# Kernel tuning notes

Measured on AMD Instinct MI355X. Metric: run time of the kernel, lower is better.

The kernel has to match this reference:

```python
import jax, jax.numpy as jnp
import numpy as np

D_MODEL = 1024
HEADS = 16
D_K = D_MODEL // HEADS
THETA = 10000.0
NEG = -1.0e9


def _rope(t, offset=0):
    # t: [B, H, S, D]; standard interleaved rotary embedding, base THETA
    S, D = t.shape[-2], t.shape[-1]
    half = D // 2
    inv_freq = 1.0 / (THETA ** (jnp.arange(half, dtype=jnp.float32) * 2.0 / D))
    pos = jnp.arange(offset, offset + S, dtype=jnp.float32)
    ang = pos[:, None] * inv_freq[None, :]          # [S, half]
    cos, sin = jnp.cos(ang), jnp.sin(ang)
    t1, t2 = t[..., ::2], t[..., 1::2]              # even / odd lanes
    o1 = t1 * cos - t2 * sin
    o2 = t1 * sin + t2 * cos
    return jnp.stack([o1, o2], axis=-1).reshape(t.shape)


def setup_inputs() -> dict:
    key = jax.random.key(0)
    k0, k1, k2, k3, k4 = jax.random.split(key, 5)
    B, S = 2, 2048
    x = jax.random.normal(k0, (B, S, D_MODEL), dtype=jnp.float32)
    att_mask = jnp.ones((B, S), dtype=jnp.int32)
    scale = 0.02
    wq = jax.random.normal(k1, (D_MODEL, D_MODEL), dtype=jnp.float32) * scale
    wk = jax.random.normal(k2, (D_MODEL, D_MODEL), dtype=jnp.float32) * scale
    wv = jax.random.normal(k3, (D_MODEL, D_MODEL), dtype=jnp.float32) * scale
    wo = jax.random.normal(k4, (D_MODEL, D_MODEL), dtype=jnp.float32) * scale
    return {"x": x, "att_mask": att_mask, "wq": wq, "wk": wk, "wv": wv, "wo": wo}


def reference(x, att_mask, wq, wk, wv, wo):
    B, S, _ = x.shape
    # nn.Linear(bias=False): y = x @ W^T ; then split heads -> [B, H, S, d_k]
    q = (x @ wq.T).reshape(B, S, HEADS, D_K).transpose(0, 2, 1, 3)
    k = (x @ wk.T).reshape(B, S, HEADS, D_K).transpose(0, 2, 1, 3)
    v = (x @ wv.T).reshape(B, S, HEADS, D_K).transpose(0, 2, 1, 3)
    # use_rope=True, start_pos=0, use_cache=False path
    q = _rope(q)
    k = _rope(k)
    scores = jnp.einsum("bhqd,bhkd->bhqk", q, k) / np.sqrt(D_K).astype(np.float32)
    pad = (att_mask == 0)[:, None, None, :]          # [B,1,1,S]
    scores = jnp.where(pad, NEG, scores)
    causal = jnp.tril(jnp.ones((S, S), dtype=bool))  # [S, S]
    scores = jnp.where(causal, scores, NEG)
    att = jax.nn.softmax(scores, axis=-1)
    ctx = jnp.einsum("bhqk,bhkd->bhqd", att, v)      # [B,H,S,d_k]
    final = ctx.transpose(0, 2, 1, 3).reshape(B, S, HEADS * D_K)
    return final @ wo.T
```

## Files before the change

kernel.cpp:

```cpp
#include <hip/hip_runtime.h>
#include <hip/hip_bf16.h>
#include <cstdint>

typedef unsigned short u16;
typedef __bf16 bf16x8 __attribute__((ext_vector_type(8)));
typedef float f32x4 __attribute__((ext_vector_type(4)));

#define S_LEN 2048
#define NH 16
#define DK 64
#define DM 1024

__device__ __forceinline__ u16 f2bf(float f) {
  union { float f; uint32_t u; } c; c.f = f;
  uint32_t u = c.u;
  u += 0x7fffu + ((u >> 16) & 1u);
  return (u16)(u >> 16);
}

__device__ __forceinline__ void gl_lds16(const void* gsrc, void* ldst) {
  __builtin_amdgcn_global_load_lds(
      (const __attribute__((address_space(1))) unsigned int*)gsrc,
      (__attribute__((address_space(3))) unsigned int*)ldst,
      16, 0, 0);
}

#define MFMA16(a, b, c) __builtin_amdgcn_mfma_f32_16x16x32_bf16((a), (b), (c), 0, 0, 0)
#define VMW(N) asm volatile("s_waitcnt vmcnt(" #N ")" ::: "memory")
#define BARM() asm volatile("s_barrier" ::: "memory")

__global__ __launch_bounds__(256) void convert_all(
    const float* x, const float* wq, const float* wk, const float* wv, const float* wo,
    u16* xb, u16* wqb, u16* wkb, u16* wvb, u16* wob)
{
  size_t i = ((size_t)blockIdx.x * 256 + threadIdx.x) * 4;
  const float* src; u16* dst; size_t off;
  if (i < 4194304u)      { src = x;  dst = xb;  off = i; }
  else if (i < 5242880u) { src = wq; dst = wqb; off = i - 4194304u; }
  else if (i < 6291456u) { src = wk; dst = wkb; off = i - 5242880u; }
  else if (i < 7340032u) { src = wv; dst = wvb; off = i - 6291456u; }
  else                   { src = wo; dst = wob; off = i - 7340032u; }
  float4 v = *(const float4*)(src + off);
  ushort4 o;
  o.x = f2bf(v.x); o.y = f2bf(v.y); o.z = f2bf(v.z); o.w = f2bf(v.w);
  *(ushort4*)(dst + off) = o;
}

__global__ __launch_bounds__(256) void rope_tab_k(float2* tab) {
  int i = blockIdx.x * 256 + threadIdx.x;
  int pos = i >> 5, f = i & 31;
  float inv = powf(10000.0f, -(float)f / 32.0f);
  float ang = (float)pos * inv;
  tab[i] = make_float2(cosf(ang), sinf(ang));
}

__global__ __launch_bounds__(64) void mask_flags(const int* amask, int* mflag) {
  const int f = blockIdx.x;
  const int b = f >> 5, t = f & 31;
  int v = amask[b * S_LEN + t * 64 + threadIdx.x];
  int all = (int)__all(v != 0);
  if (threadIdx.x == 0) mflag[f] = all;
}

__global__ __launch_bounds__(512, 2) void gemm_qkv8(
    const u16* xb, const u16* wqb, const u16* wkb, const u16* wvb,
    const float2* tab, u16* Qr, u16* Kr, u16* Vt)
{
  __shared__ __align__(16) u16 lds[2][2][2][128 * 64];

  const int bid = blockIdx.x;
  const int xcd = bid & 7, v = bid >> 3;
  const int mt = xcd * 2 + (v >= 12 ? 1 : 0);
  const int nt = (v >= 12) ? v - 12 : v;
  const int m0 = mt * 256;
  const int z = nt >> 2;
  const int n0z = (nt & 3) * 256;
  const u16* Wz = (z == 0) ? wqb : ((z == 1) ? wkb : wvb);

  const int tid = threadIdx.x;
  const int w8 = tid >> 6, lane = tid & 63;
  const int wm = w8 >> 2, wn = w8 & 3;
  const int l15 = lane & 15, g = lane >> 4;
  const int swb = ((lane & 7) * 16) ^ (((lane >> 3) & 7) << 4);

  f32x4 acc[8][4] = {};
  bf16x8 aF[2][4][2];
  bf16x8 bC[2][2];

  auto stageA = [&](int buf, int h, int kt) {
#pragma unroll
    for (int i = 0; i < 2; ++i) {
      const int rb = i * 64 + w8 * 8;
      const int row = rb + (lane >> 3);
      gl_lds16((const char*)(xb + (size_t)(m0 + h * 128 + row) * DM + kt * 64) + swb,
               (char*)&lds[buf][0][h][0] + rb * 128);
    }
  };
  auto stageB = [&](int buf, int h, int kt) {
#pragma unroll
    for (int i = 0; i < 2; ++i) {
      const int rb = i * 64 + w8 * 8;
      const int row = rb + (lane >> 3);
      gl_lds16((const char*)(Wz + (size_t)(n0z + h * 128 + row) * DM + kt * 64) + swb,
               (char*)&lds[buf][1][h][0] + rb * 128);
    }
  };
  auto loadA = [&](int cur, int mi) {
#pragma unroll
    for (int f = 0; f < 4; ++f) {
      const int row = wm * 64 + f * 16 + l15;
#pragma unroll
      for (int kk = 0; kk < 2; ++kk)
        aF[mi][f][kk] = *(const bf16x8*)((const char*)&lds[cur][0][mi][0] + row * 128 +
                                         ((kk * 64 + g * 16) ^ ((row & 7) << 4)));
    }
  };
  auto loadB = [&](int cur, int ni) {
#pragma unroll
    for (int f = 0; f < 2; ++f) {
      const int row = wn * 32 + f * 16 + l15;
#pragma unroll
      for (int kk = 0; kk < 2; ++kk)
        bC[f][kk] = *(const bf16x8*)((const char*)&lds[cur][1][ni][0] + row * 128 +
                                     ((kk * 64 + g * 16) ^ ((row & 7) << 4)));
    }
  };
  auto quad = [&](int mi, int ni) {
    __builtin_amdgcn_s_setprio(1);
#pragma unroll
    for (int f = 0; f < 4; ++f)
#pragma unroll
      for (int f2 = 0; f2 < 2; ++f2)
#pragma unroll
        for (int kk = 0; kk < 2; ++kk)
          acc[mi * 4 + f][ni * 2 + f2] =
              MFMA16(aF[mi][f][kk], bC[f2][kk], acc[mi * 4 + f][ni * 2 + f2]);
    __builtin_amdgcn_s_setprio(0);
  };

  stageA(0, 0, 0); stageB(0, 0, 0); stageA(0, 1, 0); stageB(0, 1, 0);

  for (int kt = 0; kt < 16; ++kt) {
    const int cur = kt & 1, nx = cur ^ 1;
    const bool pf = (kt < 15);
    if (pf) { stageA(nx, 0, kt + 1); VMW(6); } else { VMW(4); }
    BARM();
    loadA(cur, 0); loadB(cur, 0);
    quad(0, 0);
    if (pf) { stageB(nx, 0, kt + 1); VMW(6); } else { VMW(2); }
    BARM();
    loadA(cur, 1);
    quad(1, 0);
    if (pf) { stageA(nx, 1, kt + 1); VMW(6); } else { VMW(0); }
    BARM();
    loadB(cur, 1);
    quad(0, 1);
    if (pf) { stageB(nx, 1, kt + 1); VMW(6); }
    BARM();
    quad(1, 1);
  }

#pragma unroll
  for (int fm = 0; fm < 8; ++fm) {
    const int mrow = m0 + (fm >> 2) * 128 + wm * 64 + (fm & 3) * 16 + g * 4;
#pragma unroll
    for (int fn = 0; fn < 4; ++fn) {
      const int col = n0z + (fn >> 1) * 128 + wn * 32 + (fn & 1) * 16 + l15;
      const int h = col >> 6, d = col & 63;
#pragma unroll
      for (int r = 0; r < 4; ++r) {
        const int m = mrow + r;
        const int b = m >> 11, s = m & 2047;
        float vv = acc[fm][fn][r];
        if (z < 2) {
          float p = __shfl_xor(vv, 1);
          float2 cs = tab[s * 32 + (d >> 1)];
          float o = vv * cs.x + ((d & 1) ? p : -p) * cs.y;
          if (z == 0) o *= 0.125f;
          u16* dst = (z == 0) ? Qr : Kr;
          dst[((size_t)(b * NH + h) * S_LEN + s) * DK + d] = f2bf(o);
        } else {
          Vt[((size_t)(b * NH + h) * DK + d) * S_LEN + s] = f2bf(vv);
        }
      }
    }
  }
}

__device__ __forceinline__ void xcd_map(int bid, int& m0, int& n0) {
  const int xcd = bid & 7, v = bid >> 3;
  m0 = (xcd * 4 + (v >> 3)) * 128;
  n0 = (v & 7) * 128;
}

__global__ __launch_bounds__(256) void gemm_out(const u16* ctx, const u16* wob, float* out) {
  __shared__ __align__(16) u16 ldsA[2][128 * 64];
  __shared__ __align__(16) u16 ldsB[2][128 * 64];
  int m0, n0;
  xcd_map(blockIdx.x, m0, n0);

  const int tid = threadIdx.x;
  const int w = tid >> 6, lane = tid & 63;
  const int l15 = lane & 15, g = lane >> 4;
  const int wm = (w >> 1) * 64, wn = (w & 1) * 64;
  const int lrow = lane >> 3;
  const int scolb = ((lane & 7) * 16) ^ (lrow << 4);
  f32x4 acc[4][4] = {};

  auto stage = [&](int buf, int kt) {
#pragma unroll
    for (int c = 0; c < 4; ++c) {
      const int rb = w * 32 + c * 8;
      const int row = rb + lrow;
      gl_lds16((const char*)(ctx + (size_t)(m0 + row) * DM + kt) + scolb,
               (char*)&ldsA[buf][0] + rb * 128);
      gl_lds16((const char*)(wob + (size_t)(n0 + row) * DM + kt) + scolb,
               (char*)&ldsB[buf][0] + rb * 128);
    }
  };

  stage(0, 0);
  int cur = 0;
  for (int kt = 0; kt < DM; kt += 64) {
    if (kt + 64 < DM) { stage(cur ^ 1, kt + 64); VMW(8); } else { VMW(0); }
    BARM();
#pragma unroll
    for (int ks = 0; ks < 2; ++ks) {
      bf16x8 af[4], bfr[4];
#pragma unroll
      for (int i = 0; i < 4; ++i) {
        const int ar = wm + i * 16 + l15;
        af[i] = *(const bf16x8*)((const char*)&ldsA[cur][0] + ar * 128 +
                                 ((ks * 64 + g * 16) ^ ((ar & 7) << 4)));
        const int br = wn + i * 16 + l15;
        bfr[i] = *(const bf16x8*)((const char*)&ldsB[cur][0] + br * 128 +
                                  ((ks * 64 + g * 16) ^ ((br & 7) << 4)));
      }
      __builtin_amdgcn_s_setprio(1);
#pragma unroll
      for (int i = 0; i < 4; ++i)
#pragma unroll
        for (int j = 0; j < 4; ++j)
          acc[i][j] = MFMA16(af[i], bfr[j], acc[i][j]);
      __builtin_amdgcn_s_setprio(0);
    }
    BARM();
    cur ^= 1;
  }

#pragma unroll
  for (int i = 0; i < 4; ++i)
#pragma unroll
    for (int j = 0; j < 4; ++j)
#pragma unroll
      for (int r = 0; r < 4; ++r)
        out[(size_t)(m0 + wm + i * 16 + g * 4 + r) * DM + n0 + wn + j * 16 + l15] = acc[i][j][r];
}

__global__ __launch_bounds__(512, 4) void attn9(
    const u16* Qr, const u16* Kr, const u16* Vt, const int* amask, const int* mflag,
    u16* ctx)
{
  __shared__ __align__(16) u16 ldsK[2][64 * 64];
  __shared__ __align__(16) u16 ldsV[2][64 * 64];
  __shared__ __align__(16) __bf16 plds[8][16 * 72];

  const int bh = blockIdx.x;
  const int grp = 15 - blockIdx.y;
  const int b = bh >> 4, h = bh & 15;
  const int tid = threadIdx.x, w8 = tid >> 6, lane = tid & 63;
  const int l15 = lane & 15, g = lane >> 4;
  const int r8 = lane >> 3;
  const int sw = ((lane & 7) * 16) ^ (r8 << 4);

  const int chunk = grp * 4 + (w8 >> 1);
  const int q0 = chunk * 32 + (w8 & 1) * 16;
  const int myNt = (chunk >> 1) + 1;
  const int dTile = chunk >> 1;
  const int ntB = grp * 2 + 2;

  const u16* Kb0 = Kr + (size_t)bh * S_LEN * DK;
  const u16* Vb0 = Vt + (size_t)bh * DK * S_LEN;
  const u16* Qb  = Qr + (size_t)bh * S_LEN * DK;

  bf16x8 qa0 = *(const bf16x8*)(Qb + (size_t)(q0 + l15) * DK + g * 8);
  bf16x8 qa1 = *(const bf16x8*)(Qb + (size_t)(q0 + l15) * DK + 32 + g * 8);

  union { u16 u[8]; bf16x8 v; } one_u;
#pragma unroll
  for (int i = 0; i < 8; ++i) one_u.u[i] = 0x3F80;
  const bf16x8 ones = one_u.v;

  float m[4];
  f32x4 lacc = {0.f, 0.f, 0.f, 0.f};
  f32x4 o[4];
#pragma unroll
  for (int r = 0; r < 4; ++r) m[r] = -3e38f;
#pragma unroll
  for (int dt = 0; dt < 4; ++dt) o[dt] = (f32x4){0.f, 0.f, 0.f, 0.f};

  auto stage = [&](int buf, int t) {
    const size_t kv0 = (size_t)t * 64;
    const int row = w8 * 8 + r8;
    gl_lds16((const char*)(Kb0 + (kv0 + row) * DK) + sw,
             (char*)&ldsK[buf][0] + (w8 * 8) * 128);
    gl_lds16((const char*)(Vb0 + (size_t)row * S_LEN + kv0) + sw,
             (char*)&ldsV[buf][0] + (w8 * 8) * 128);
  };

  stage(0, 0);
  int cur = 0;

  for (int t = 0; t < ntB; ++t) {
    if (t + 1 < ntB) { stage(cur ^ 1, t + 1); VMW(2); } else { VMW(0); }
    BARM();
    if (t < myNt) {
      const int kv0 = t * 64;
      const bool allok = mflag[(b << 5) + t] != 0;

      bf16x8 kb[4][2];
#pragma unroll
      for (int nt = 0; nt < 4; ++nt) {
        const int row = nt * 16 + l15;
#pragma unroll
        for (int ks = 0; ks < 2; ++ks)
          kb[nt][ks] = *(const bf16x8*)((const char*)&ldsK[cur][0] + row * 128 +
                                        ((ks * 64 + g * 16) ^ ((row & 7) << 4)));
      }
      f32x4 s[4];
#pragma unroll
      for (int nt = 0; nt < 4; ++nt) s[nt] = (f32x4){0.f, 0.f, 0.f, 0.f};
      __builtin_amdgcn_s_setprio(1);
#pragma unroll
      for (int nt = 0; nt < 4; ++nt) {
        s[nt] = MFMA16(qa0, kb[nt][0], s[nt]);
        s[nt] = MFMA16(qa1, kb[nt][1], s[nt]);
      }
      __builtin_amdgcn_s_setprio(0);

      if (!allok) {
#pragma unroll
        for (int nt = 0; nt < 4; ++nt) {
          const int pmv = amask[b * S_LEN + kv0 + nt * 16 + l15];
#pragma unroll
          for (int r = 0; r < 4; ++r)
            if (!pmv) s[nt][r] = -1e9f;
        }
      }
      if (t == dTile) {
#pragma unroll
        for (int nt = 0; nt < 4; ++nt) {
          const int kvc = kv0 + nt * 16 + l15;
#pragma unroll
          for (int r = 0; r < 4; ++r)
            s[nt][r] = (kvc <= q0 + g * 4 + r) ? s[nt][r] : -1e9f;
        }
      }

      float tmax[4];
      bool need = false;
#pragma unroll
      for (int r = 0; r < 4; ++r) {
        float t0 = fmaxf(fmaxf(s[0][r], s[1][r]), fmaxf(s[2][r], s[3][r]));
        t0 = fmaxf(t0, __shfl_xor(t0, 1));
        t0 = fmaxf(t0, __shfl_xor(t0, 2));
        t0 = fmaxf(t0, __shfl_xor(t0, 4));
        t0 = fmaxf(t0, __shfl_xor(t0, 8));
        tmax[r] = t0;
        need = need || (t0 > m[r] + 8.f);
      }
      if (__any((int)need)) {
#pragma unroll
        for (int r = 0; r < 4; ++r) {
          const float mnew = fmaxf(m[r], tmax[r]);
          const float alpha = __expf(m[r] - mnew);
          m[r] = mnew;
          lacc[r] *= alpha;
#pragma unroll
          for (int dt = 0; dt < 4; ++dt) o[dt][r] *= alpha;
        }
      }
      __bf16* pw = &plds[w8][0];
#pragma unroll
      for (int r = 0; r < 4; ++r) {
#pragma unroll
        for (int nt = 0; nt < 4; ++nt)
          pw[(g * 4 + r) * 72 + nt * 16 + l15] = (__bf16)__expf(s[nt][r] - m[r]);
      }
      bf16x8 pa0 = *(const bf16x8*)(pw + l15 * 72 + g * 8);
      bf16x8 pa1 = *(const bf16x8*)(pw + l15 * 72 + 32 + g * 8);
      bf16x8 vb[4][2];
#pragma unroll
      for (int dt = 0; dt < 4; ++dt) {
        const int row = dt * 16 + l15;
#pragma unroll
        for (int ks = 0; ks < 2; ++ks)
          vb[dt][ks] = *(const bf16x8*)((const char*)&ldsV[cur][0] + row * 128 +
                                        ((ks * 64 + g * 16) ^ ((row & 7) << 4)));
      }
      __builtin_amdgcn_s_setprio(1);
      lacc = MFMA16(pa0, ones, lacc);
      lacc = MFMA16(pa1, ones, lacc);
#pragma unroll
      for (int dt = 0; dt < 4; ++dt) {
        o[dt] = MFMA16(pa0, vb[dt][0], o[dt]);
        o[dt] = MFMA16(pa1, vb[dt][1], o[dt]);
      }
      __builtin_amdgcn_s_setprio(0);
    }
    BARM();
    cur ^= 1;
  }

#pragma unroll
  for (int dt = 0; dt < 4; ++dt)
#pragma unroll
    for (int r = 0; r < 4; ++r) {
      const int q = q0 + g * 4 + r;
      ctx[((size_t)(b * S_LEN + q)) * DM + h * DK + dt * 16 + l15] =
          f2bf(o[dt][r] / lacc[r]);
    }
}

extern "C" void kernel_launch(void* const* d_in, const int* in_sizes, int n_in,
                              void* d_out, int out_size, void* d_ws, size_t ws_size,
                              hipStream_t stream) {
  const float* x   = (const float*)d_in[0];
  const int* amask = (const int*)d_in[1];
  const float* wq  = (const float*)d_in[2];
  const float* wk  = (const float*)d_in[3];
  const float* wv  = (const float*)d_in[4];
  const float* wo  = (const float*)d_in[5];
  float* out = (float*)d_out;

  char* ws = (char*)d_ws;
  u16* xb    = (u16*)(ws);
  u16* wqb   = (u16*)(ws + ( 8u << 20));
  u16* wkb   = (u16*)(ws + (10u << 20));
  u16* wvb   = (u16*)(ws + (12u << 20));
  u16* wob   = (u16*)(ws + (14u << 20));
  float2* tab = (float2*)(ws + (16u << 20));
  int* mflag = (int*)(ws + (16u << 20) + (768u << 10));
  u16* Qr    = (u16*)(ws + (17u << 20));
  u16* Kr    = (u16*)(ws + (25u << 20));
  u16* Vt    = (u16*)(ws + (33u << 20));
  u16* ctx   = (u16*)(ws + (41u << 20));

  hipLaunchKernelGGL(convert_all, dim3(8192), dim3(256), 0, stream,
                     x, wq, wk, wv, wo, xb, wqb, wkb, wvb, wob);
  hipLaunchKernelGGL(rope_tab_k, dim3(256), dim3(256), 0, stream, tab);
  hipLaunchKernelGGL(mask_flags, dim3(64), dim3(64), 0, stream, amask, mflag);
  hipLaunchKernelGGL(gemm_qkv8, dim3(192), dim3(512), 0, stream,
                     xb, wqb, wkb, wvb, tab, Qr, Kr, Vt);
  hipLaunchKernelGGL(attn9, dim3(32, 16), dim3(512), 0, stream,
                     Qr, Kr, Vt, amask, mflag, ctx);
  hipLaunchKernelGGL(gemm_out, dim3(256), dim3(256), 0, stream, ctx, wob, out);
}
```

Measured before the change: 149.9 us.

## Use 128x128 tiles for QKV GEMM and 32-row query blocks per attention wave

The QKV projection changes from 256x256 tiles on 512-thread blocks (192 blocks) to 128x128 tiles on 256-thread blocks (768 blocks), reusing the gemm_out main loop. Attention moves from 8 waves of 16 query rows each to 4 waves of 32 query rows each, so every K/V fragment loaded from LDS feeds two query sets. The aim is better K/V reuse in attention and better CU fill in the GEMM. In exchange, each GEMM block reuses less data per tile, and attention needs more registers per wave and runs fewer waves.

New measurement: 178.1 us. 1.19x slower.

```diff
diff --git a/kernel.cpp b/kernel.cpp
--- a/kernel.cpp
+++ b/kernel.cpp
@@ -62,142 +62,20 @@
   if (threadIdx.x == 0) mflag[f] = all;
 }
 
-__global__ __launch_bounds__(512, 2) void gemm_qkv8(
+__global__ __launch_bounds__(256) void gemm_qkv128(
     const u16* xb, const u16* wqb, const u16* wkb, const u16* wvb,
     const float2* tab, u16* Qr, u16* Kr, u16* Vt)
 {
-  __shared__ __align__(16) u16 lds[2][2][2][128 * 64];
+  __shared__ __align__(16) u16 ldsA[2][128 * 64];
+  __shared__ __align__(16) u16 ldsB[2][128 * 64];
 
   const int bid = blockIdx.x;
   const int xcd = bid & 7, v = bid >> 3;
-  const int mt = xcd * 2 + (v >= 12 ? 1 : 0);
-  const int nt = (v >= 12) ? v - 12 : v;
-  const int m0 = mt * 256;
-  const int z = nt >> 2;
-  const int n0z = (nt & 3) * 256;
+  const int m0 = (xcd * 4 + (v & 3)) * 128;
+  const int nc = v >> 2;
+  const int z = nc >> 3;
+  const int n0z = (nc & 7) * 128;
   const u16* Wz = (z == 0) ? wqb : ((z == 1) ? wkb : wvb);
-
-  const int tid = threadIdx.x;
-  const int w8 = tid >> 6, lane = tid & 63;
-  const int wm = w8 >> 2, wn = w8 & 3;
-  const int l15 = lane & 15, g = lane >> 4;
-  const int swb = ((lane & 7) * 16) ^ (((lane >> 3) & 7) << 4);
-
-  f32x4 acc[8][4] = {};
-  bf16x8 aF[2][4][2];
-  bf16x8 bC[2][2];
-
-  auto stageA = [&](int buf, int h, int kt) {
-#pragma unroll
-    for (int i = 0; i < 2; ++i) {
-      const int rb = i * 64 + w8 * 8;
-      const int row = rb + (lane >> 3);
-      gl_lds16((const char*)(xb + (size_t)(m0 + h * 128 + row) * DM + kt * 64) + swb,
-               (char*)&lds[buf][0][h][0] + rb * 128);
-    }
-  };
-  auto stageB = [&](int buf, int h, int kt) {
-#pragma unroll
-    for (int i = 0; i < 2; ++i) {
-      const int rb = i * 64 + w8 * 8;
-      const int row = rb + (lane >> 3);
-      gl_lds16((const char*)(Wz + (size_t)(n0z + h * 128 + row) * DM + kt * 64) + swb,
-               (char*)&lds[buf][1][h][0] + rb * 128);
-    }
-  };
-  auto loadA = [&](int cur, int mi) {
-#pragma unroll
-    for (int f = 0; f < 4; ++f) {
-      const int row = wm * 64 + f * 16 + l15;
-#pragma unroll
-      for (int kk = 0; kk < 2; ++kk)
-        aF[mi][f][kk] = *(const bf16x8*)((const char*)&lds[cur][0][mi][0] + row * 128 +
-                                         ((kk * 64 + g * 16) ^ ((row & 7) << 4)));
-    }
-  };
-  auto loadB = [&](int cur, int ni) {
-#pragma unroll
-    for (int f = 0; f < 2; ++f) {
-      const int row = wn * 32 + f * 16 + l15;
-#pragma unroll
-      for (int kk = 0; kk < 2; ++kk)
-        bC[f][kk] = *(const bf16x8*)((const char*)&lds[cur][1][ni][0] + row * 128 +
-                                     ((kk * 64 + g * 16) ^ ((row & 7) << 4)));
-    }
-  };
-  auto quad = [&](int mi, int ni) {
-    __builtin_amdgcn_s_setprio(1);
-#pragma unroll
-    for (int f = 0; f < 4; ++f)
-#pragma unroll
-      for (int f2 = 0; f2 < 2; ++f2)
-#pragma unroll
-        for (int kk = 0; kk < 2; ++kk)
-          acc[mi * 4 + f][ni * 2 + f2] =
-              MFMA16(aF[mi][f][kk], bC[f2][kk], acc[mi * 4 + f][ni * 2 + f2]);
-    __builtin_amdgcn_s_setprio(0);
-  };
-
-  stageA(0, 0, 0); stageB(0, 0, 0); stageA(0, 1, 0); stageB(0, 1, 0);
-
-  for (int kt = 0; kt < 16; ++kt) {
-    const int cur = kt & 1, nx = cur ^ 1;
-    const bool pf = (kt < 15);
-    if (pf) { stageA(nx, 0, kt + 1); VMW(6); } else { VMW(4); }
-    BARM();
-    loadA(cur, 0); loadB(cur, 0);
-    quad(0, 0);
-    if (pf) { stageB(nx, 0, kt + 1); VMW(6); } else { VMW(2); }
-    BARM();
-    loadA(cur, 1);
-    quad(1, 0);
-    if (pf) { stageA(nx, 1, kt + 1); VMW(6); } else { VMW(0); }
-    BARM();
-    loadB(cur, 1);
-    quad(0, 1);
-    if (pf) { stageB(nx, 1, kt + 1); VMW(6); }
-    BARM();
-    quad(1, 1);
-  }
-
-#pragma unroll
-  for (int fm = 0; fm < 8; ++fm) {
-    const int mrow = m0 + (fm >> 2) * 128 + wm * 64 + (fm & 3) * 16 + g * 4;
-#pragma unroll
-    for (int fn = 0; fn < 4; ++fn) {
-      const int col = n0z + (fn >> 1) * 128 + wn * 32 + (fn & 1) * 16 + l15;
-      const int h = col >> 6, d = col & 63;
-#pragma unroll
-      for (int r = 0; r < 4; ++r) {
-        const int m = mrow + r;
-        const int b = m >> 11, s = m & 2047;
-        float vv = acc[fm][fn][r];
-        if (z < 2) {
-          float p = __shfl_xor(vv, 1);
-          float2 cs = tab[s * 32 + (d >> 1)];
-          float o = vv * cs.x + ((d & 1) ? p : -p) * cs.y;
-          if (z == 0) o *= 0.125f;
-          u16* dst = (z == 0) ? Qr : Kr;
-          dst[((size_t)(b * NH + h) * S_LEN + s) * DK + d] = f2bf(o);
-        } else {
-          Vt[((size_t)(b * NH + h) * DK + d) * S_LEN + s] = f2bf(vv);
-        }
-      }
-    }
-  }
-}
-
-__device__ __forceinline__ void xcd_map(int bid, int& m0, int& n0) {
-  const int xcd = bid & 7, v = bid >> 3;
-  m0 = (xcd * 4 + (v >> 3)) * 128;
-  n0 = (v & 7) * 128;
-}
-
-__global__ __launch_bounds__(256) void gemm_out(const u16* ctx, const u16* wob, float* out) {
-  __shared__ __align__(16) u16 ldsA[2][128 * 64];
-  __shared__ __align__(16) u16 ldsB[2][128 * 64];
-  int m0, n0;
-  xcd_map(blockIdx.x, m0, n0);
 
   const int tid = threadIdx.x;
   const int w = tid >> 6, lane = tid & 63;
@@ -212,9 +90,9 @@
     for (int c = 0; c < 4; ++c) {
       const int rb = w * 32 + c * 8;
       const int row = rb + lrow;
-      gl_lds16((const char*)(ctx + (size_t)(m0 + row) * DM + kt) + scolb,
+      gl_lds16((const char*)(xb + (size_t)(m0 + row) * DM + kt) + scolb,
                (char*)&ldsA[buf][0] + rb * 128);
-      gl_lds16((const char*)(wob + (size_t)(n0 + row) * DM + kt) + scolb,
+      gl_lds16((const char*)(Wz + (size_t)(n0z + row) * DM + kt) + scolb,
                (char*)&ldsB[buf][0] + rb * 128);
     }
   };
@@ -248,6 +126,93 @@
     cur ^= 1;
   }
 
+  u16* dst = (z == 0) ? Qr : Kr;
+#pragma unroll
+  for (int i = 0; i < 4; ++i) {
+#pragma unroll
+    for (int j = 0; j < 4; ++j) {
+      const int n = n0z + wn + j * 16 + l15;
+      const int h = n >> 6, d = n & 63;
+#pragma unroll
+      for (int r = 0; r < 4; ++r) {
+        const int m = m0 + wm + i * 16 + g * 4 + r;
+        const int b = m >> 11, s = m & 2047;
+        float vv = acc[i][j][r];
+        if (z < 2) {
+          float p = __shfl_xor(vv, 1);
+          float2 cs = tab[s * 32 + (d >> 1)];
+          float o = vv * cs.x + ((d & 1) ? p : -p) * cs.y;
+          if (z == 0) o *= 0.125f;
+          dst[((size_t)(b * NH + h) * S_LEN + s) * DK + d] = f2bf(o);
+        } else {
+          Vt[((size_t)(b * NH + h) * DK + d) * S_LEN + s] = f2bf(vv);
+        }
+      }
+    }
+  }
+}
+
+__device__ __forceinline__ void xcd_map(int bid, int& m0, int& n0) {
+  const int xcd = bid & 7, v = bid >> 3;
+  m0 = (xcd * 4 + (v >> 3)) * 128;
+  n0 = (v & 7) * 128;
+}
+
+__global__ __launch_bounds__(256) void gemm_out(const u16* ctx, const u16* wob, float* out) {
+  __shared__ __align__(16) u16 ldsA[2][128 * 64];
+  __shared__ __align__(16) u16 ldsB[2][128 * 64];
+  int m0, n0;
+  xcd_map(blockIdx.x, m0, n0);
+
+  const int tid = threadIdx.x;
+  const int w = tid >> 6, lane = tid & 63;
+  const int l15 = lane & 15, g = lane >> 4;
+  const int wm = (w >> 1) * 64, wn = (w & 1) * 64;
+  const int lrow = lane >> 3;
+  const int scolb = ((lane & 7) * 16) ^ (lrow << 4);
+  f32x4 acc[4][4] = {};
+
+  auto stage = [&](int buf, int kt) {
+#pragma unroll
+    for (int c = 0; c < 4; ++c) {
+      const int rb = w * 32 + c * 8;
+      const int row = rb + lrow;
+      gl_lds16((const char*)(ctx + (size_t)(m0 + row) * DM + kt) + scolb,
+               (char*)&ldsA[buf][0] + rb * 128);
+      gl_lds16((const char*)(wob + (size_t)(n0 + row) * DM + kt) + scolb,
+               (char*)&ldsB[buf][0] + rb * 128);
+    }
+  };
+
+  stage(0, 0);
+  int cur = 0;
+  for (int kt = 0; kt < DM; kt += 64) {
+    if (kt + 64 < DM) { stage(cur ^ 1, kt + 64); VMW(8); } else { VMW(0); }
+    BARM();
+#pragma unroll
+    for (int ks = 0; ks < 2; ++ks) {
+      bf16x8 af[4], bfr[4];
+#pragma unroll
+      for (int i = 0; i < 4; ++i) {
+        const int ar = wm + i * 16 + l15;
+        af[i] = *(const bf16x8*)((const char*)&ldsA[cur][0] + ar * 128 +
+                                 ((ks * 64 + g * 16) ^ ((ar & 7) << 4)));
+        const int br = wn + i * 16 + l15;
+        bfr[i] = *(const bf16x8*)((const char*)&ldsB[cur][0] + br * 128 +
+                                  ((ks * 64 + g * 16) ^ ((br & 7) << 4)));
+      }
+      __builtin_amdgcn_s_setprio(1);
+#pragma unroll
+      for (int i = 0; i < 4; ++i)
+#pragma unroll
+        for (int j = 0; j < 4; ++j)
+          acc[i][j] = MFMA16(af[i], bfr[j], acc[i][j]);
+      __builtin_amdgcn_s_setprio(0);
+    }
+    BARM();
+    cur ^= 1;
+  }
+
 #pragma unroll
   for (int i = 0; i < 4; ++i)
 #pragma unroll
@@ -257,62 +222,73 @@
         out[(size_t)(m0 + wm + i * 16 + g * 4 + r) * DM + n0 + wn + j * 16 + l15] = acc[i][j][r];
 }
 
-__global__ __launch_bounds__(512, 4) void attn9(
+__global__ __launch_bounds__(256) void attn10(
     const u16* Qr, const u16* Kr, const u16* Vt, const int* amask, const int* mflag,
     u16* ctx)
 {
   __shared__ __align__(16) u16 ldsK[2][64 * 64];
   __shared__ __align__(16) u16 ldsV[2][64 * 64];
-  __shared__ __align__(16) __bf16 plds[8][16 * 72];
+  __shared__ __align__(16) __bf16 plds[4][32 * 72];
 
   const int bh = blockIdx.x;
-  const int grp = 15 - blockIdx.y;
+  const int band = 15 - blockIdx.y;
   const int b = bh >> 4, h = bh & 15;
-  const int tid = threadIdx.x, w8 = tid >> 6, lane = tid & 63;
+  const int tid = threadIdx.x, w = tid >> 6, lane = tid & 63;
   const int l15 = lane & 15, g = lane >> 4;
   const int r8 = lane >> 3;
   const int sw = ((lane & 7) * 16) ^ (r8 << 4);
 
-  const int chunk = grp * 4 + (w8 >> 1);
-  const int q0 = chunk * 32 + (w8 & 1) * 16;
+  const int chunk = band * 4 + w;
+  const int q0 = chunk * 32;
   const int myNt = (chunk >> 1) + 1;
   const int dTile = chunk >> 1;
-  const int ntB = grp * 2 + 2;
+  const int ntB = band * 2 + 2;
 
   const u16* Kb0 = Kr + (size_t)bh * S_LEN * DK;
   const u16* Vb0 = Vt + (size_t)bh * DK * S_LEN;
   const u16* Qb  = Qr + (size_t)bh * S_LEN * DK;
 
-  bf16x8 qa0 = *(const bf16x8*)(Qb + (size_t)(q0 + l15) * DK + g * 8);
-  bf16x8 qa1 = *(const bf16x8*)(Qb + (size_t)(q0 + l15) * DK + 32 + g * 8);
+  bf16x8 qa[2][2];
+#pragma unroll
+  for (int set = 0; set < 2; ++set) {
+    qa[set][0] = *(const bf16x8*)(Qb + (size_t)(q0 + set * 16 + l15) * DK + g * 8);
+    qa[set][1] = *(const bf16x8*)(Qb + (size_t)(q0 + set * 16 + l15) * DK + 32 + g * 8);
+  }
 
   union { u16 u[8]; bf16x8 v; } one_u;
 #pragma unroll
   for (int i = 0; i < 8; ++i) one_u.u[i] = 0x3F80;
   const bf16x8 ones = one_u.v;
 
-  float m[4];
-  f32x4 lacc = {0.f, 0.f, 0.f, 0.f};
-  f32x4 o[4];
-#pragma unroll
-  for (int r = 0; r < 4; ++r) m[r] = -3e38f;
-#pragma unroll
-  for (int dt = 0; dt < 4; ++dt) o[dt] = (f32x4){0.f, 0.f, 0.f, 0.f};
+  float m[2][4];
+  f32x4 lacc[2] = {{0.f, 0.f, 0.f, 0.f}, {0.f, 0.f, 0.f, 0.f}};
+  f32x4 o[2][4];
+#pragma unroll
+  for (int set = 0; set < 2; ++set) {
+#pragma unroll
+    for (int r = 0; r < 4; ++r) m[set][r] = -3e38f;
+#pragma unroll
+    for (int dt = 0; dt < 4; ++dt) o[set][dt] = (f32x4){0.f, 0.f, 0.f, 0.f};
+  }
 
   auto stage = [&](int buf, int t) {
     const size_t kv0 = (size_t)t * 64;
-    const int row = w8 * 8 + r8;
-    gl_lds16((const char*)(Kb0 + (kv0 + row) * DK) + sw,
-             (char*)&ldsK[buf][0] + (w8 * 8) * 128);
-    gl_lds16((const char*)(Vb0 + (size_t)row * S_LEN + kv0) + sw,
-             (char*)&ldsV[buf][0] + (w8 * 8) * 128);
+#pragma unroll
+    for (int i = 0; i < 2; ++i) {
+      const int rb = w * 16 + i * 8;
+      const int row = rb + r8;
+      gl_lds16((const char*)(Kb0 + (kv0 + row) * DK) + sw,
+               (char*)&ldsK[buf][0] + rb * 128);
+      gl_lds16((const char*)(Vb0 + (size_t)row * S_LEN + kv0) + sw,
+               (char*)&ldsV[buf][0] + rb * 128);
+    }
   };
 
   stage(0, 0);
   int cur = 0;
 
   for (int t = 0; t < ntB; ++t) {
-    if (t + 1 < ntB) { stage(cur ^ 1, t + 1); VMW(2); } else { VMW(0); }
+    if (t + 1 < ntB) { stage(cur ^ 1, t + 1); VMW(4); } else { VMW(0); }
     BARM();
     if (t < myNt) {
       const int kv0 = t * 64;
@@ -327,68 +303,73 @@
           kb[nt][ks] = *(const bf16x8*)((const char*)&ldsK[cur][0] + row * 128 +
                                         ((ks * 64 + g * 16) ^ ((row & 7) << 4)));
       }
-      f32x4 s[4];
-#pragma unroll
-      for (int nt = 0; nt < 4; ++nt) s[nt] = (f32x4){0.f, 0.f, 0.f, 0.f};
-      __builtin_amdgcn_s_setprio(1);
-#pragma unroll
-      for (int nt = 0; nt < 4; ++nt) {
-        s[nt] = MFMA16(qa0, kb[nt][0], s[nt]);
-        s[nt] = MFMA16(qa1, kb[nt][1], s[nt]);
-      }
-      __builtin_amdgcn_s_setprio(0);
-
-      if (!allok) {
+      __bf16* pw = &plds[w][0];
+
+#pragma unroll
+      for (int set = 0; set < 2; ++set) {
+        f32x4 s[4];
+#pragma unroll
+        for (int nt = 0; nt < 4; ++nt) s[nt] = (f32x4){0.f, 0.f, 0.f, 0.f};
+        __builtin_amdgcn_s_setprio(1);
 #pragma unroll
         for (int nt = 0; nt < 4; ++nt) {
-          const int pmv = amask[b * S_LEN + kv0 + nt * 16 + l15];
-#pragma unroll
-          for (int r = 0; r < 4; ++r)
-            if (!pmv) s[nt][r] = -1e9f;
-        }
-      }
-      if (t == dTile) {
-#pragma unroll
-        for (int nt = 0; nt < 4; ++nt) {
-          const int kvc = kv0 + nt * 16 + l15;
-#pragma unroll
-          for (int r = 0; r < 4; ++r)
-            s[nt][r] = (kvc <= q0 + g * 4 + r) ? s[nt][r] : -1e9f;
-        }
-      }
-
-      float tmax[4];
-      bool need = false;
-#pragma unroll
-      for (int r = 0; r < 4; ++r) {
-        float t0 = fmaxf(fmaxf(s[0][r], s[1][r]), fmaxf(s[2][r], s[3][r]));
-        t0 = fmaxf(t0, __shfl_xor(t0, 1));
-        t0 = fmaxf(t0, __shfl_xor(t0, 2));
-        t0 = fmaxf(t0, __shfl_xor(t0, 4));
-        t0 = fmaxf(t0, __shfl_xor(t0, 8));
-        tmax[r] = t0;
-        need = need || (t0 > m[r] + 8.f);
-      }
-      if (__any((int)need)) {
+          s[nt] = MFMA16(qa[set][0], kb[nt][0], s[nt]);
+          s[nt] = MFMA16(qa[set][1], kb[nt][1], s[nt]);
+        }
+        __builtin_amdgcn_s_setprio(0);
+
+        if (!allok) {
+#pragma unroll
+          for (int nt = 0; nt < 4; ++nt) {
+            const int pmv = amask[b * S_LEN + kv0 + nt * 16 + l15];
+#pragma unroll
+            for (int r = 0; r < 4; ++r)
+              if (!pmv) s[nt][r] = -1e9f;
+          }
+        }
+        if (t == dTile) {
+          const int qrow0 = q0 + set * 16 + g * 4;
+#pragma unroll
+          for (int nt = 0; nt < 4; ++nt) {
+            const int kvc = kv0 + nt * 16 + l15;
+#pragma unroll
+            for (int r = 0; r < 4; ++r)
+              s[nt][r] = (kvc <= qrow0 + r) ? s[nt][r] : -1e9f;
+          }
+        }
+
+        float tmax[4];
+        bool need = false;
 #pragma unroll
         for (int r = 0; r < 4; ++r) {
-          const float mnew = fmaxf(m[r], tmax[r]);
-          const float alpha = __expf(m[r] - mnew);
-          m[r] = mnew;
-          lacc[r] *= alpha;
-#pragma unroll
-          for (int dt = 0; dt < 4; ++dt) o[dt][r] *= alpha;
-        }
-      }
-      __bf16* pw = &plds[w8][0];
-#pragma unroll
-      for (int r = 0; r < 4; ++r) {
-#pragma unroll
-        for (int nt = 0; nt < 4; ++nt)
-          pw[(g * 4 + r) * 72 + nt * 16 + l15] = (__bf16)__expf(s[nt][r] - m[r]);
-      }
-      bf16x8 pa0 = *(const bf16x8*)(pw + l15 * 72 + g * 8);
-      bf16x8 pa1 = *(const bf16x8*)(pw + l15 * 72 + 32 + g * 8);
+          float t0 = fmaxf(fmaxf(s[0][r], s[1][r]), fmaxf(s[2][r], s[3][r]));
+          t0 = fmaxf(t0, __shfl_xor(t0, 1));
+          t0 = fmaxf(t0, __shfl_xor(t0, 2));
+          t0 = fmaxf(t0, __shfl_xor(t0, 4));
+          t0 = fmaxf(t0, __shfl_xor(t0, 8));
+          tmax[r] = t0;
+          need = need || (t0 > m[set][r] + 8.f);
+        }
+        if (__any((int)need)) {
+#pragma unroll
+          for (int r = 0; r < 4; ++r) {
+            const float mnew = fmaxf(m[set][r], tmax[r]);
+            const float alpha = __expf(m[set][r] - mnew);
+            m[set][r] = mnew;
+            lacc[set][r] *= alpha;
+#pragma unroll
+            for (int dt = 0; dt < 4; ++dt) o[set][dt][r] *= alpha;
+          }
+        }
+#pragma unroll
+        for (int r = 0; r < 4; ++r) {
+#pragma unroll
+          for (int nt = 0; nt < 4; ++nt)
+            pw[(set * 16 + g * 4 + r) * 72 + nt * 16 + l15] =
+                (__bf16)__expf(s[nt][r] - m[set][r]);
+        }
+      }
+
       bf16x8 vb[4][2];
 #pragma unroll
       for (int dt = 0; dt < 4; ++dt) {
@@ -398,28 +379,35 @@
           vb[dt][ks] = *(const bf16x8*)((const char*)&ldsV[cur][0] + row * 128 +
                                         ((ks * 64 + g * 16) ^ ((row & 7) << 4)));
       }
-      __builtin_amdgcn_s_setprio(1);
-      lacc = MFMA16(pa0, ones, lacc);
-      lacc = MFMA16(pa1, ones, lacc);
-#pragma unroll
-      for (int dt = 0; dt < 4; ++dt) {
-        o[dt] = MFMA16(pa0, vb[dt][0], o[dt]);
-        o[dt] = MFMA16(pa1, vb[dt][1], o[dt]);
-      }
-      __builtin_amdgcn_s_setprio(0);
+#pragma unroll
+      for (int set = 0; set < 2; ++set) {
+        bf16x8 pa0 = *(const bf16x8*)(pw + (set * 16 + l15) * 72 + g * 8);
+        bf16x8 pa1 = *(const bf16x8*)(pw + (set * 16 + l15) * 72 + 32 + g * 8);
+        __builtin_amdgcn_s_setprio(1);
+        lacc[set] = MFMA16(pa0, ones, lacc[set]);
+        lacc[set] = MFMA16(pa1, ones, lacc[set]);
+#pragma unroll
+        for (int dt = 0; dt < 4; ++dt) {
+          o[set][dt] = MFMA16(pa0, vb[dt][0], o[set][dt]);
+          o[set][dt] = MFMA16(pa1, vb[dt][1], o[set][dt]);
+        }
+        __builtin_amdgcn_s_setprio(0);
+      }
     }
     BARM();
     cur ^= 1;
   }
 
 #pragma unroll
-  for (int dt = 0; dt < 4; ++dt)
-#pragma unroll
-    for (int r = 0; r < 4; ++r) {
-      const int q = q0 + g * 4 + r;
-      ctx[((size_t)(b * S_LEN + q)) * DM + h * DK + dt * 16 + l15] =
-          f2bf(o[dt][r] / lacc[r]);
-    }
+  for (int set = 0; set < 2; ++set)
+#pragma unroll
+    for (int dt = 0; dt < 4; ++dt)
+#pragma unroll
+      for (int r = 0; r < 4; ++r) {
+        const int q = q0 + set * 16 + g * 4 + r;
+        ctx[((size_t)(b * S_LEN + q)) * DM + h * DK + dt * 16 + l15] =
+            f2bf(o[set][dt][r] / lacc[set][r]);
+      }
 }
 
 extern "C" void kernel_launch(void* const* d_in, const int* in_sizes, int n_in,
@@ -450,9 +438,9 @@
                      x, wq, wk, wv, wo, xb, wqb, wkb, wvb, wob);
   hipLaunchKernelGGL(rope_tab_k, dim3(256), dim3(256), 0, stream, tab);
   hipLaunchKernelGGL(mask_flags, dim3(64), dim3(64), 0, stream, amask, mflag);
-  hipLaunchKernelGGL(gemm_qkv8, dim3(192), dim3(512), 0, stream,
+  hipLaunchKernelGGL(gemm_qkv128, dim3(768), dim3(256), 0, stream,
                      xb, wqb, wkb, wvb, tab, Qr, Kr, Vt);
-  hipLaunchKernelGGL(attn9, dim3(32, 16), dim3(512), 0, stream,
+  hipLaunchKernelGGL(attn10, dim3(32, 16), dim3(256), 0, stream,
                      Qr, Kr, Vt, amask, mflag, ctx);
   hipLaunchKernelGGL(gemm_out, dim3(256), dim3(256), 0, stream, ctx, wob, out);
 }
```

## Restructure QKV GEMM into 8-phase pipelined 256-tile and reorder attention bands

Applied to the files above, without the earlier changes.

The QKV projection GEMM moves into a helper that stages full 256-row A and B tiles into double-buffered LDS. It uses an 8-phase schedule that prefetches B two k-steps ahead and interleaves LDS loads, global-to-LDS copies and MFMA quads between barriers. Each wave's N layout changes from 128-column halves to contiguous 64-column slices. The XCD-aware block mapping is replaced by a simple mt/nt split, and attention blocks now alternate heavy causal bands with light ones for better load balance. The new schedule adds more barriers per k-step and drops the L2 locality of the old XCD mapping.

Measured after the change: 157.7 us. 5.2% more time.

```diff
diff --git a/kernel.cpp b/kernel.cpp
--- a/kernel.cpp
+++ b/kernel.cpp
@@ -62,114 +62,133 @@
   if (threadIdx.x == 0) mflag[f] = all;
 }
 
-__global__ __launch_bounds__(512, 2) void gemm_qkv8(
-    const u16* xb, const u16* wqb, const u16* wkb, const u16* wvb,
-    const float2* tab, u16* Qr, u16* Kr, u16* Vt)
+__device__ __forceinline__ void gemm256_8ph(
+    const u16* A, const u16* Bp, int m0, int n0,
+    u16 (&ldsA)[2][256 * 64], u16 (&ldsB)[2][256 * 64], f32x4 (&acc)[8][4])
 {
-  __shared__ __align__(16) u16 lds[2][2][2][128 * 64];
-
-  const int bid = blockIdx.x;
-  const int xcd = bid & 7, v = bid >> 3;
-  const int mt = xcd * 2 + (v >= 12 ? 1 : 0);
-  const int nt = (v >= 12) ? v - 12 : v;
-  const int m0 = mt * 256;
-  const int z = nt >> 2;
-  const int n0z = (nt & 3) * 256;
-  const u16* Wz = (z == 0) ? wqb : ((z == 1) ? wkb : wvb);
-
   const int tid = threadIdx.x;
   const int w8 = tid >> 6, lane = tid & 63;
   const int wm = w8 >> 2, wn = w8 & 3;
   const int l15 = lane & 15, g = lane >> 4;
   const int swb = ((lane & 7) * 16) ^ (((lane >> 3) & 7) << 4);
 
+  bf16x8 aF[4][2];
+  bf16x8 bF[2][2][2];
+
+  auto stA = [&](int buf, int kt, int c0) {
+#pragma unroll
+    for (int c = 0; c < 2; ++c) {
+      const int rb = (c0 + c) * 64 + w8 * 8;
+      const int row = rb + (lane >> 3);
+      gl_lds16((const char*)(A + (size_t)(m0 + row) * DM + kt * 64) + swb,
+               (char*)&ldsA[buf][0] + rb * 128);
+    }
+  };
+  auto stB = [&](int buf, int kt, int c0) {
+#pragma unroll
+    for (int c = 0; c < 2; ++c) {
+      const int rb = (c0 + c) * 64 + w8 * 8;
+      const int row = rb + (lane >> 3);
+      gl_lds16((const char*)(Bp + (size_t)(n0 + row) * DM + kt * 64) + swb,
+               (char*)&ldsB[buf][0] + rb * 128);
+    }
+  };
+  auto ldA = [&](int cur, int qm) {
+#pragma unroll
+    for (int f = 0; f < 4; ++f) {
+      const int row = qm * 128 + wm * 64 + f * 16 + l15;
+#pragma unroll
+      for (int kk = 0; kk < 2; ++kk)
+        aF[f][kk] = *(const bf16x8*)((const char*)&ldsA[cur][0] + row * 128 +
+                                     ((kk * 64 + g * 16) ^ ((row & 7) << 4)));
+    }
+  };
+  auto ldB = [&](int cur, int qn) {
+#pragma unroll
+    for (int f2 = 0; f2 < 2; ++f2) {
+      const int row = wn * 64 + qn * 32 + f2 * 16 + l15;
+#pragma unroll
+      for (int kk = 0; kk < 2; ++kk)
+        bF[qn][f2][kk] = *(const bf16x8*)((const char*)&ldsB[cur][0] + row * 128 +
+                                          ((kk * 64 + g * 16) ^ ((row & 7) << 4)));
+    }
+  };
+  auto quad = [&](int qm, int qn) {
+    __builtin_amdgcn_s_setprio(1);
+#pragma unroll
+    for (int f = 0; f < 4; ++f)
+#pragma unroll
+      for (int f2 = 0; f2 < 2; ++f2)
+#pragma unroll
+        for (int kk = 0; kk < 2; ++kk)
+          acc[qm * 4 + f][qn * 2 + f2] =
+              MFMA16(aF[f][kk], bF[qn][f2][kk], acc[qm * 4 + f][qn * 2 + f2]);
+    __builtin_amdgcn_s_setprio(0);
+  };
+
+  stB(0, 0, 0); stB(0, 0, 2);
+  stA(0, 0, 0); stA(0, 0, 2);
+  stB(1, 1, 0); stB(1, 1, 2);
+  VMW(4);
+  BARM();
+
+  for (int t = 0; t < 16; ++t) {
+    const int cur = t & 1, nx = cur ^ 1;
+    ldA(cur, 0); ldB(cur, 0);
+    if (t < 15) stA(nx, t + 1, 0);
+    BARM();
+    quad(0, 0);
+    BARM();
+    ldB(cur, 1);
+    if (t < 15) stA(nx, t + 1, 2);
+    BARM();
+    quad(0, 1);
+    BARM();
+    ldA(cur, 1);
+    if (t < 14) stB(cur, t + 2, 0);
+    BARM();
+    quad(1, 0);
+    BARM();
+    if (t < 14) stB(cur, t + 2, 2);
+    BARM();
+    quad(1, 1);
+    if (t < 14) { VMW(4); } else if (t == 14) { VMW(0); }
+    BARM();
+  }
+}
+
+__global__ __launch_bounds__(512, 2) void gemm_qkv256(
+    const u16* xb, const u16* wqb, const u16* wkb, const u16* wvb,
+    const float2* tab, u16* Qr, u16* Kr, u16* Vt)
+{
+  __shared__ __align__(16) u16 ldsA[2][256 * 64];
+  __shared__ __align__(16) u16 ldsB[2][256 * 64];
+
+  const int bid = blockIdx.x;
+  const int mt = bid & 15, nt = bid >> 4;
+  const int m0 = mt * 256;
+  const int z = nt >> 2;
+  const int n0z = (nt & 3) * 256;
+  const u16* Wz = (z == 0) ? wqb : ((z == 1) ? wkb : wvb);
+
   f32x4 acc[8][4] = {};
-  bf16x8 aF[2][4][2];
-  bf16x8 bC[2][2];
-
-  auto stageA = [&](int buf, int h, int kt) {
-#pragma unroll
-    for (int i = 0; i < 2; ++i) {
-      const int rb = i * 64 + w8 * 8;
-      const int row = rb + (lane >> 3);
-      gl_lds16((const char*)(xb + (size_t)(m0 + h * 128 + row) * DM + kt * 64) + swb,
-               (char*)&lds[buf][0][h][0] + rb * 128);
-    }
-  };
-  auto stageB = [&](int buf, int h, int kt) {
-#pragma unroll
-    for (int i = 0; i < 2; ++i) {
-      const int rb = i * 64 + w8 * 8;
-      const int row = rb + (lane >> 3);
-      gl_lds16((const char*)(Wz + (size_t)(n0z + h * 128 + row) * DM + kt * 64) + swb,
-               (char*)&lds[buf][1][h][0] + rb * 128);
-    }
-  };
-  auto loadA = [&](int cur, int mi) {
-#pragma unroll
-    for (int f = 0; f < 4; ++f) {
-      const int row = wm * 64 + f * 16 + l15;
-#pragma unroll
-      for (int kk = 0; kk < 2; ++kk)
-        aF[mi][f][kk] = *(const bf16x8*)((const char*)&lds[cur][0][mi][0] + row * 128 +
-                                         ((kk * 64 + g * 16) ^ ((row & 7) << 4)));
-    }
-  };
-  auto loadB = [&](int cur, int ni) {
-#pragma unroll
-    for (int f = 0; f < 2; ++f) {
-      const int row = wn * 32 + f * 16 + l15;
-#pragma unroll
-      for (int kk = 0; kk < 2; ++kk)
-        bC[f][kk] = *(const bf16x8*)((const char*)&lds[cur][1][ni][0] + row * 128 +
-                                     ((kk * 64 + g * 16) ^ ((row & 7) << 4)));
-    }
-  };
-  auto quad = [&](int mi, int ni) {
-    __builtin_amdgcn_s_setprio(1);
-#pragma unroll
-    for (int f = 0; f < 4; ++f)
-#pragma unroll
-      for (int f2 = 0; f2 < 2; ++f2)
-#pragma unroll
-        for (int kk = 0; kk < 2; ++kk)
-          acc[mi * 4 + f][ni * 2 + f2] =
-              MFMA16(aF[mi][f][kk], bC[f2][kk], acc[mi * 4 + f][ni * 2 + f2]);
-    __builtin_amdgcn_s_setprio(0);
-  };
-
-  stageA(0, 0, 0); stageB(0, 0, 0); stageA(0, 1, 0); stageB(0, 1, 0);
-
-  for (int kt = 0; kt < 16; ++kt) {
-    const int cur = kt & 1, nx = cur ^ 1;
-    const bool pf = (kt < 15);
-    if (pf) { stageA(nx, 0, kt + 1); VMW(6); } else { VMW(4); }
-    BARM();
-    loadA(cur, 0); loadB(cur, 0);
-    quad(0, 0);
-    if (pf) { stageB(nx, 0, kt + 1); VMW(6); } else { VMW(2); }
-    BARM();
-    loadA(cur, 1);
-    quad(1, 0);
-    if (pf) { stageA(nx, 1, kt + 1); VMW(6); } else { VMW(0); }
-    BARM();
-    loadB(cur, 1);
-    quad(0, 1);
-    if (pf) { stageB(nx, 1, kt + 1); VMW(6); }
-    BARM();
-    quad(1, 1);
-  }
-
+  gemm256_8ph(xb, Wz, m0, n0z, ldsA, ldsB, acc);
+
+  const int tid = threadIdx.x;
+  const int w8 = tid >> 6, lane = tid & 63;
+  const int wm = w8 >> 2, wn = w8 & 3;
+  const int l15 = lane & 15, g = lane >> 4;
+  u16* dst = (z == 0) ? Qr : Kr;
 #pragma unroll
   for (int fm = 0; fm < 8; ++fm) {
-    const int mrow = m0 + (fm >> 2) * 128 + wm * 64 + (fm & 3) * 16 + g * 4;
+    const int row0 = m0 + (fm >> 2) * 128 + wm * 64 + (fm & 3) * 16 + g * 4;
 #pragma unroll
     for (int fn = 0; fn < 4; ++fn) {
-      const int col = n0z + (fn >> 1) * 128 + wn * 32 + (fn & 1) * 16 + l15;
+      const int col = n0z + wn * 64 + (fn >> 1) * 32 + (fn & 1) * 16 + l15;
       const int h = col >> 6, d = col & 63;
 #pragma unroll
       for (int r = 0; r < 4; ++r) {
-        const int m = mrow + r;
+        const int m = row0 + r;
         const int b = m >> 11, s = m & 2047;
         float vv = acc[fm][fn][r];
         if (z < 2) {
@@ -177,7 +196,6 @@
           float2 cs = tab[s * 32 + (d >> 1)];
           float o = vv * cs.x + ((d & 1) ? p : -p) * cs.y;
           if (z == 0) o *= 0.125f;
-          u16* dst = (z == 0) ? Qr : Kr;
           dst[((size_t)(b * NH + h) * S_LEN + s) * DK + d] = f2bf(o);
         } else {
           Vt[((size_t)(b * NH + h) * DK + d) * S_LEN + s] = f2bf(vv);
@@ -257,7 +275,7 @@
         out[(size_t)(m0 + wm + i * 16 + g * 4 + r) * DM + n0 + wn + j * 16 + l15] = acc[i][j][r];
 }
 
-__global__ __launch_bounds__(512, 4) void attn9(
+__global__ __launch_bounds__(512, 4) void attn11(
     const u16* Qr, const u16* Kr, const u16* Vt, const int* amask, const int* mflag,
     u16* ctx)
 {
@@ -266,18 +284,19 @@
   __shared__ __align__(16) __bf16 plds[8][16 * 72];
 
   const int bh = blockIdx.x;
-  const int grp = 15 - blockIdx.y;
+  const int by = blockIdx.y;
+  const int band = (by < 8) ? (15 - by) : (by - 8);
   const int b = bh >> 4, h = bh & 15;
   const int tid = threadIdx.x, w8 = tid >> 6, lane = tid & 63;
   const int l15 = lane & 15, g = lane >> 4;
   const int r8 = lane >> 3;
   const int sw = ((lane & 7) * 16) ^ (r8 << 4);
 
-  const int chunk = grp * 4 + (w8 >> 1);
+  const int chunk = band * 4 + (w8 >> 1);
   const int q0 = chunk * 32 + (w8 & 1) * 16;
   const int myNt = (chunk >> 1) + 1;
   const int dTile = chunk >> 1;
-  const int ntB = grp * 2 + 2;
+  const int ntB = band * 2 + 2;
 
   const u16* Kb0 = Kr + (size_t)bh * S_LEN * DK;
   const u16* Vb0 = Vt + (size_t)bh * DK * S_LEN;
@@ -450,9 +469,9 @@
                      x, wq, wk, wv, wo, xb, wqb, wkb, wvb, wob);
   hipLaunchKernelGGL(rope_tab_k, dim3(256), dim3(256), 0, stream, tab);
   hipLaunchKernelGGL(mask_flags, dim3(64), dim3(64), 0, stream, amask, mflag);
-  hipLaunchKernelGGL(gemm_qkv8, dim3(192), dim3(512), 0, stream,
+  hipLaunchKernelGGL(gemm_qkv256, dim3(192), dim3(512), 0, stream,
                      xb, wqb, wkb, wvb, tab, Qr, Kr, Vt);
-  hipLaunchKernelGGL(attn9, dim3(32, 16), dim3(512), 0, stream,
+  hipLaunchKernelGGL(attn11, dim3(32, 16), dim3(512), 0, stream,
                      Qr, Kr, Vt, amask, mflag, ctx);
   hipLaunchKernelGGL(gemm_out, dim3(256), dim3(256), 0, stream, ctx, wob, out);
 }
```
